# Performance work log

Hardware: AMD Instinct MI355X
Metric: run time of the kernel (lower is better)

## Reference

```python
import jax, jax.numpy as jnp
import numpy as np

N_NODES = 100000
N_EDGES = 1600000
IN_CH, HID, OUT_CH = 512, 16, 64


def setup_inputs() -> dict:
    key = jax.random.key(0)
    ks = jax.random.split(key, 9)
    x = jax.random.normal(ks[0], (N_NODES, IN_CH), dtype=jnp.float32)
    edge_index1 = jax.random.randint(ks[1], (2, N_EDGES), 0, N_NODES, dtype=jnp.int32)
    edge_weight1 = jax.random.uniform(ks[2], (N_EDGES,), dtype=jnp.float32)
    edge_index2 = jax.random.randint(ks[3], (2, N_EDGES), 0, N_NODES, dtype=jnp.int32)
    edge_weight2 = jax.random.uniform(ks[4], (N_EDGES,), dtype=jnp.float32)
    W1 = jax.random.normal(ks[5], (IN_CH, HID), dtype=jnp.float32) / np.sqrt(IN_CH)
    b1 = jnp.zeros((HID,), dtype=jnp.float32)
    W2 = jax.random.normal(ks[6], (HID, OUT_CH), dtype=jnp.float32) / np.sqrt(HID)
    b2 = jnp.zeros((OUT_CH,), dtype=jnp.float32)
    return dict(x=x, edge_index1=edge_index1, edge_weight1=edge_weight1,
                edge_index2=edge_index2, edge_weight2=edge_weight2,
                W1=W1, b1=b1, W2=W2, b2=b2, num_nodes=N_NODES)


def _gcn_conv(x, W, b, row, col, w, num_nodes):
    # symmetric-normalized GCN aggregation: out = D^-1/2 A D^-1/2 (x W) + b
    deg = jax.ops.segment_sum(w, row, num_segments=num_nodes)  # [N]
    dinv = jnp.where(deg > 0, jax.lax.rsqrt(jnp.maximum(deg, 1e-12)), 0.0)
    norm = dinv[row] * w * dinv[col]                            # [E]
    h = x @ W                                                   # [N, F_out]
    msg = norm[:, None] * h[col]                                # [E, F_out]
    return jax.ops.segment_sum(msg, row, num_segments=num_nodes) + b


def reference(x, edge_index1, edge_weight1, edge_index2, edge_weight2,
              W1, b1, W2, b2, num_nodes):
    # concat edge lists; torch_sparse.coalesce(op='add') merges duplicates by
    # summing weights — the subsequent degree + scatter-add aggregation is
    # invariant to that dedup, so we run directly on the concatenated list.
    ei = jnp.concatenate([edge_index1, edge_index2], axis=1)    # [2, 2E]
    ew = jnp.concatenate([edge_weight1, edge_weight2])          # [2E]
    row, col = ei[0], ei[1]
    h = _gcn_conv(x, W1, b1, row, col, ew, num_nodes)
    h = jax.nn.relu(h)  # dropout is identity in eval mode
    h = _gcn_conv(h, W2, b2, row, col, ew, num_nodes)
    return jax.nn.log_softmax(h, axis=1)
```

## Files before the change

### kernel.cpp

```cpp
#include <hip/hip_runtime.h>
#include <hip/hip_bf16.h>

#define IN_CH 512
#define HID 16
#define OUT_CH 64
#define CAP 20480

typedef __attribute__((ext_vector_type(8))) short bf16x8;
typedef __attribute__((ext_vector_type(4))) float f32x4;

__device__ inline unsigned short f2bf(float f) {
    unsigned int u = __float_as_uint(f);
    return (unsigned short)((u + 0x7fffu + ((u >> 16) & 1u)) >> 16);
}

union A8 { bf16x8 v; short2 p[4]; };
__device__ inline short2 pk2(float a, float b) {
    union { __hip_bfloat162 h; short2 s; } u;
    u.h = __float22bfloat162_rn(make_float2(a, b));
    return u.s;
}

__global__ void k_init(int* __restrict__ cursors, int nbk) {
    int i = threadIdx.x;
    if (i < nbk) cursors[i] = i * CAP;
}

__global__ __launch_bounds__(1024) void k_partition(const int* __restrict__ ei1, const float* __restrict__ w1, int E1,
                                                    const int* __restrict__ ei2, const float* __restrict__ w2, int E2,
                                                    int* __restrict__ cursors,
                                                    uint2* __restrict__ packed, int Et) {
    __shared__ int hist[256];
    __shared__ int cur[256];
    int tid = threadIdx.x;
    if (tid < 256) hist[tid] = 0;
    __syncthreads();
    int e0 = blockIdx.x * 16384 + tid;
    #pragma unroll
    for (int j = 0; j < 16; ++j) {
        int e = e0 + j * 1024;
        if (e < Et) {
            int r = (e < E1) ? ei1[e] : ei2[e - E1];
            atomicAdd(&hist[r >> 9], 1);
        }
    }
    __syncthreads();
    if (tid < 256) {
        int h = hist[tid];
        cur[tid] = (h > 0) ? atomicAdd(&cursors[tid], h) : 0;
    }
    __syncthreads();
    #pragma unroll
    for (int j = 0; j < 16; ++j) {
        int e = e0 + j * 1024;
        if (e < Et) {
            int r, c; float w;
            if (e < E1) { r = ei1[e]; c = ei1[e + E1]; w = w1[e]; }
            else        { int f = e - E1; r = ei2[f]; c = ei2[f + E2]; w = w2[f]; }
            int b = r >> 9;
            int pos = atomicAdd(&cur[b], 1);
            packed[pos] = make_uint2(((unsigned)(r & 511) << 17) | (unsigned)c,
                                     __float_as_uint(w));
        }
    }
}

__global__ void k_bucket_scan(const int* __restrict__ cursors, int* __restrict__ cbase, int nbk) {
    __shared__ int s[256];
    int tid = threadIdx.x;
    int v = (tid < nbk) ? (cursors[tid] - tid * CAP) : 0;
    s[tid] = v;
    __syncthreads();
    for (int off = 1; off < 256; off <<= 1) {
        int t = (tid >= off) ? s[tid - off] : 0;
        __syncthreads();
        s[tid] += t;
        __syncthreads();
    }
    if (tid < nbk) cbase[tid] = s[tid] - v;
}

__global__ __launch_bounds__(1024) void k_buildcsr(const uint2* __restrict__ packed,
                                                   const int* __restrict__ cursors,
                                                   const int* __restrict__ cbase,
                                                   int* __restrict__ rowstart, int* __restrict__ cnt,
                                                   float* __restrict__ dinv, int2* __restrict__ csr, int N) {
    __shared__ int lcnt[512];
    __shared__ int lcur[512];
    __shared__ int lscan[512];
    __shared__ float ldeg[512];
    int b = blockIdx.x, tid = threadIdx.x;
    int M = cursors[b] - b * CAP;
    const uint2* pk = packed + (size_t)b * CAP;
    if (tid < 512) { lcnt[tid] = 0; ldeg[tid] = 0.f; }
    __syncthreads();
    for (int i = tid; i < M; i += 1024) atomicAdd(&lcnt[pk[i].x >> 17], 1);
    __syncthreads();
    int v = (tid < 512) ? lcnt[tid] : 0;
    if (tid < 512) lscan[tid] = v;
    __syncthreads();
    for (int off = 1; off < 512; off <<= 1) {
        int t = (tid >= off && tid < 512) ? lscan[tid - off] : 0;
        __syncthreads();
        if (tid < 512) lscan[tid] += t;
        __syncthreads();
    }
    int cb = cbase[b];
    if (tid < 512) {
        int ex = lscan[tid] - v;
        lcur[tid] = cb + ex;
        int node = b * 512 + tid;
        if (node < N) { rowstart[node] = cb + ex; cnt[node] = v; }
    }
    __syncthreads();
    for (int i = tid; i < M; i += 1024) {
        uint2 u = pk[i];
        int lr = u.x >> 17;
        int c  = u.x & 0x1FFFF;
        int p = atomicAdd(&lcur[lr], 1);
        csr[p] = make_int2(c, (int)u.y);
        atomicAdd(&ldeg[lr], __uint_as_float(u.y));
    }
    __syncthreads();
    if (tid < 512) {
        int node = b * 512 + tid;
        if (node < N) {
            float d = ldeg[tid];
            dinv[node] = (d > 0.f) ? rsqrtf(fmaxf(d, 1e-12f)) : 0.f;
        }
    }
}

__global__ void k_prep(const float* __restrict__ W1, unsigned short* __restrict__ W1s) {
    for (int p = threadIdx.x; p < 1024; p += 256) {
        int kc = p >> 6, lane = p & 63;
        int q = lane >> 4, m = lane & 15;
        int k0 = kc * 32 + q * 8;
        unsigned v[8];
        #pragma unroll
        for (int j = 0; j < 8; ++j) v[j] = f2bf(W1[(k0 + j) * HID + m]);
        uint4 o;
        o.x = v[0] | (v[1] << 16); o.y = v[2] | (v[3] << 16);
        o.z = v[4] | (v[5] << 16); o.w = v[6] | (v[7] << 16);
        ((uint4*)W1s)[p] = o;
    }
}

__global__ __launch_bounds__(256) void k_gemm1(const float* __restrict__ x,
                                               const unsigned short* __restrict__ W1s,
                                               const float* __restrict__ dinv,
                                               float* __restrict__ h1s, int n) {
    int wave = threadIdx.x >> 6, lane = threadIdx.x & 63;
    int tiles = (n + 15) >> 4;
    int t = blockIdx.x * 4 + wave;
    if (t >= tiles) return;

    int m = lane & 15, quad = lane >> 4;

    const bf16x8* Wv = (const bf16x8*)W1s;
    bf16x8 Bf[16];
    #pragma unroll
    for (int kc = 0; kc < 16; ++kc) Bf[kc] = Wv[kc * 64 + lane];

    int row = t * 16 + m;
    int rl = min(row, n - 1);
    const float4* xr = (const float4*)(x + (size_t)rl * IN_CH + quad * 8);

    f32x4 acc = {0.f, 0.f, 0.f, 0.f};
    #pragma unroll
    for (int kc = 0; kc < 16; ++kc) {
        float4 v0 = xr[kc * 8];
        float4 v1 = xr[kc * 8 + 1];
        A8 a;
        a.p[0] = pk2(v0.x, v0.y); a.p[1] = pk2(v0.z, v0.w);
        a.p[2] = pk2(v1.x, v1.y); a.p[3] = pk2(v1.z, v1.w);
        acc = __builtin_amdgcn_mfma_f32_16x16x32_bf16(a.v, Bf[kc], acc, 0, 0, 0);
    }

    int base = t * 16 + quad * 4;
    #pragma unroll
    for (int r = 0; r < 4; ++r) {
        int orow = base + r;
        if (orow < n) h1s[(size_t)orow * HID + m] = dinv[orow] * acc[r];
    }
}

__global__ __launch_bounds__(256) void k_agg1(const float* __restrict__ h1s,
                                              const int2* __restrict__ csr,
                                              const int* __restrict__ rowstart,
                                              const int* __restrict__ cnt,
                                              const float* __restrict__ dinv,
                                              const float* __restrict__ b1,
                                              float* __restrict__ out1s, int n) {
    int wave = threadIdx.x >> 6, lane = threadIdx.x & 63;
    int node = blockIdx.x * 4 + wave;
    if (node >= n) return;
    int slot = lane >> 2, c4 = lane & 3;
    const int2* ce = csr + rowstart[node];
    int deg = cnt[node];
    f32x4 acc = {0.f, 0.f, 0.f, 0.f};
    for (int i = slot; i < deg; i += 16) {
        int2 e = ce[i];
        float w = __int_as_float(e.y);
        float4 hv = ((const float4*)(h1s + (size_t)e.x * HID))[c4];
        acc[0] = fmaf(w, hv.x, acc[0]); acc[1] = fmaf(w, hv.y, acc[1]);
        acc[2] = fmaf(w, hv.z, acc[2]); acc[3] = fmaf(w, hv.w, acc[3]);
    }
    #pragma unroll
    for (int off = 4; off < 64; off <<= 1) {
        acc[0] += __shfl_xor(acc[0], off, 64);
        acc[1] += __shfl_xor(acc[1], off, 64);
        acc[2] += __shfl_xor(acc[2], off, 64);
        acc[3] += __shfl_xor(acc[3], off, 64);
    }
    if (lane < 4) {
        float dv = dinv[node];
        float4 bb = ((const float4*)b1)[c4];
        float4 o;
        o.x = fmaxf(fmaf(dv, acc[0], bb.x), 0.f) * dv;
        o.y = fmaxf(fmaf(dv, acc[1], bb.y), 0.f) * dv;
        o.z = fmaxf(fmaf(dv, acc[2], bb.z), 0.f) * dv;
        o.w = fmaxf(fmaf(dv, acc[3], bb.w), 0.f) * dv;
        ((float4*)(out1s + (size_t)node * HID))[c4] = o;
    }
}

__global__ __launch_bounds__(256) void k_layer2(const float* __restrict__ out1s,
                                                const int2* __restrict__ csr,
                                                const int* __restrict__ rowstart,
                                                const int* __restrict__ cnt,
                                                const float* __restrict__ dinv,
                                                const float* __restrict__ W2,
                                                const float* __restrict__ b2,
                                                float* __restrict__ out, int n) {
    __shared__ float W2l[HID * OUT_CH];
    for (int i = threadIdx.x; i < HID * OUT_CH; i += 256) W2l[i] = W2[i];
    __syncthreads();

    int wave = threadIdx.x >> 6, lane = threadIdx.x & 63;
    int node = blockIdx.x * 4 + wave;
    if (node >= n) return;
    int slot = lane >> 2, c4 = lane & 3;
    const int2* ce = csr + rowstart[node];
    int deg = cnt[node];
    f32x4 acc = {0.f, 0.f, 0.f, 0.f};
    for (int i = slot; i < deg; i += 16) {
        int2 e = ce[i];
        float w = __int_as_float(e.y);
        float4 hv = ((const float4*)(out1s + (size_t)e.x * HID))[c4];
        acc[0] = fmaf(w, hv.x, acc[0]); acc[1] = fmaf(w, hv.y, acc[1]);
        acc[2] = fmaf(w, hv.z, acc[2]); acc[3] = fmaf(w, hv.w, acc[3]);
    }
    #pragma unroll
    for (int off = 4; off < 64; off <<= 1) {
        acc[0] += __shfl_xor(acc[0], off, 64);
        acc[1] += __shfl_xor(acc[1], off, 64);
        acc[2] += __shfl_xor(acc[2], off, 64);
        acc[3] += __shfl_xor(acc[3], off, 64);
    }
    float dv = dinv[node];
    acc[0] *= dv; acc[1] *= dv; acc[2] *= dv; acc[3] *= dv;
    float v = b2[lane];
    #pragma unroll
    for (int gg = 0; gg < 4; ++gg) {
        float a0 = __shfl(acc[0], gg, 64);
        float a1 = __shfl(acc[1], gg, 64);
        float a2 = __shfl(acc[2], gg, 64);
        float a3 = __shfl(acc[3], gg, 64);
        v = fmaf(a0, W2l[(4 * gg + 0) * OUT_CH + lane], v);
        v = fmaf(a1, W2l[(4 * gg + 1) * OUT_CH + lane], v);
        v = fmaf(a2, W2l[(4 * gg + 2) * OUT_CH + lane], v);
        v = fmaf(a3, W2l[(4 * gg + 3) * OUT_CH + lane], v);
    }
    float m = v;
    #pragma unroll
    for (int off = 32; off; off >>= 1) m = fmaxf(m, __shfl_xor(m, off, 64));
    float ex = __expf(v - m);
    float s = ex;
    #pragma unroll
    for (int off = 32; off; off >>= 1) s += __shfl_xor(s, off, 64);
    out[(size_t)node * OUT_CH + lane] = (v - m) - __logf(s);
}

extern "C" void kernel_launch(void* const* d_in, const int* in_sizes, int n_in,
                              void* d_out, int out_size, void* d_ws, size_t ws_size,
                              hipStream_t stream) {
    const float* x   = (const float*)d_in[0];
    const int*   ei1 = (const int*)d_in[1];
    const float* w1  = (const float*)d_in[2];
    const int*   ei2 = (const int*)d_in[3];
    const float* w2  = (const float*)d_in[4];
    const float* W1  = (const float*)d_in[5];
    const float* b1  = (const float*)d_in[6];
    const float* W2  = (const float*)d_in[7];
    const float* b2  = (const float*)d_in[8];
    int N  = in_sizes[0] / IN_CH;
    int E1 = in_sizes[2];
    int E2 = in_sizes[4];
    int Et = E1 + E2;
    float* out = (float*)d_out;
    int nbk = (N + 511) >> 9;

    char* p = (char*)d_ws;
    int*   cursors  = (int*)p;   p += 1024;
    int*   cbase    = (int*)p;   p += 1024;
    int*   rowstart = (int*)p;   p += (size_t)N * 4;
    int*   cnt      = (int*)p;   p += (size_t)N * 4;
    float* dinv     = (float*)p; p += (size_t)N * 4;
    unsigned short* W1s = (unsigned short*)p; p += IN_CH * HID * 2;
    int2*  csr      = (int2*)p;  p += (size_t)Et * 8;
    uint2* packed   = (uint2*)p;
    float* h1s      = (float*)p;
    float* out1s    = h1s + (size_t)N * HID;

    k_init<<<1, 256, 0, stream>>>(cursors, nbk);
    k_prep<<<1, 256, 0, stream>>>(W1, W1s);
    k_partition<<<(Et + 16383) / 16384, 1024, 0, stream>>>(ei1, w1, E1, ei2, w2, E2,
                                                           cursors, packed, Et);
    k_bucket_scan<<<1, 256, 0, stream>>>(cursors, cbase, nbk);
    k_buildcsr<<<nbk, 1024, 0, stream>>>(packed, cursors, cbase,
                                         rowstart, cnt, dinv, csr, N);
    int tiles = (N + 15) / 16;
    k_gemm1<<<(tiles + 3) / 4, 256, 0, stream>>>(x, W1s, dinv, h1s, N);
    k_agg1<<<(N + 3) / 4, 256, 0, stream>>>(h1s, csr, rowstart, cnt, dinv, b1, out1s, N);
    k_layer2<<<(N + 3) / 4, 256, 0, stream>>>(out1s, csr, rowstart, cnt, dinv, W2, b2, out, N);
}
```

Baseline: 539.6 us.

## Store hidden features as bf16, merge small kernels, privatize partition histogram

The intermediate hidden features h1s and out1s are now stored as bf16, which halves gather traffic in both aggregation kernels. Those kernels now use 2 lanes per edge and 32 edge slots per wave. The init and W1 prep kernels become one launch, and the bucket scan is folded into every buildcsr block, removing two launches. The partition kernel uses per-256-thread histograms and caches row indices in registers so they are not reloaded. The bf16 storage lowers accuracy of intermediates, and every buildcsr block now repeats the bucket scan.

```diff
diff --git a/kernel.cpp b/kernel.cpp
--- a/kernel.cpp
+++ b/kernel.cpp
@@ -13,6 +13,8 @@
     unsigned int u = __float_as_uint(f);
     return (unsigned short)((u + 0x7fffu + ((u >> 16) & 1u)) >> 16);
 }
+__device__ inline float blo(unsigned u) { return __uint_as_float(u << 16); }
+__device__ inline float bhi(unsigned u) { return __uint_as_float(u & 0xFFFF0000u); }
 
 union A8 { bf16x8 v; short2 p[4]; };
 __device__ inline short2 pk2(float a, float b) {
@@ -21,70 +23,76 @@
     return u.s;
 }
 
-__global__ void k_init(int* __restrict__ cursors, int nbk) {
-    int i = threadIdx.x;
-    if (i < nbk) cursors[i] = i * CAP;
+__global__ void k_init_prep(int* __restrict__ cursors, int nbk,
+                            const float* __restrict__ W1, unsigned short* __restrict__ W1s) {
+    if (blockIdx.x == 0) {
+        int i = threadIdx.x;
+        if (i < nbk) cursors[i] = i * CAP;
+    } else {
+        for (int p = threadIdx.x; p < 1024; p += 256) {
+            int kc = p >> 6, lane = p & 63;
+            int q = lane >> 4, m = lane & 15;
+            int k0 = kc * 32 + q * 8;
+            unsigned v[8];
+            #pragma unroll
+            for (int j = 0; j < 8; ++j) v[j] = f2bf(W1[(k0 + j) * HID + m]);
+            uint4 o;
+            o.x = v[0] | (v[1] << 16); o.y = v[2] | (v[3] << 16);
+            o.z = v[4] | (v[5] << 16); o.w = v[6] | (v[7] << 16);
+            ((uint4*)W1s)[p] = o;
+        }
+    }
 }
 
 __global__ __launch_bounds__(1024) void k_partition(const int* __restrict__ ei1, const float* __restrict__ w1, int E1,
                                                     const int* __restrict__ ei2, const float* __restrict__ w2, int E2,
                                                     int* __restrict__ cursors,
                                                     uint2* __restrict__ packed, int Et) {
-    __shared__ int hist[256];
+    __shared__ int hist[4][256];
     __shared__ int cur[256];
     int tid = threadIdx.x;
-    if (tid < 256) hist[tid] = 0;
+    int wg = tid >> 8;
+    if (tid < 256) { hist[0][tid] = 0; hist[1][tid] = 0; hist[2][tid] = 0; hist[3][tid] = 0; }
     __syncthreads();
     int e0 = blockIdx.x * 16384 + tid;
+    int rr[16];
     #pragma unroll
     for (int j = 0; j < 16; ++j) {
         int e = e0 + j * 1024;
+        rr[j] = -1;
         if (e < Et) {
             int r = (e < E1) ? ei1[e] : ei2[e - E1];
-            atomicAdd(&hist[r >> 9], 1);
+            rr[j] = r;
+            atomicAdd(&hist[wg][r >> 9], 1);
         }
     }
     __syncthreads();
     if (tid < 256) {
-        int h = hist[tid];
+        int h = hist[0][tid] + hist[1][tid] + hist[2][tid] + hist[3][tid];
         cur[tid] = (h > 0) ? atomicAdd(&cursors[tid], h) : 0;
     }
     __syncthreads();
     #pragma unroll
     for (int j = 0; j < 16; ++j) {
         int e = e0 + j * 1024;
-        if (e < Et) {
-            int r, c; float w;
-            if (e < E1) { r = ei1[e]; c = ei1[e + E1]; w = w1[e]; }
-            else        { int f = e - E1; r = ei2[f]; c = ei2[f + E2]; w = w2[f]; }
-            int b = r >> 9;
+        if (rr[j] >= 0) {
+            int c; float w;
+            if (e < E1) { c = ei1[e + E1]; w = w1[e]; }
+            else        { int f = e - E1; c = ei2[f + E2]; w = w2[f]; }
+            int b = rr[j] >> 9;
             int pos = atomicAdd(&cur[b], 1);
-            packed[pos] = make_uint2(((unsigned)(r & 511) << 17) | (unsigned)c,
+            packed[pos] = make_uint2(((unsigned)(rr[j] & 511) << 17) | (unsigned)c,
                                      __float_as_uint(w));
         }
     }
-}
-
-__global__ void k_bucket_scan(const int* __restrict__ cursors, int* __restrict__ cbase, int nbk) {
-    __shared__ int s[256];
-    int tid = threadIdx.x;
-    int v = (tid < nbk) ? (cursors[tid] - tid * CAP) : 0;
-    s[tid] = v;
-    __syncthreads();
-    for (int off = 1; off < 256; off <<= 1) {
-        int t = (tid >= off) ? s[tid - off] : 0;
-        __syncthreads();
-        s[tid] += t;
-        __syncthreads();
-    }
-    if (tid < nbk) cbase[tid] = s[tid] - v;
 }
 
 __global__ __launch_bounds__(1024) void k_buildcsr(const uint2* __restrict__ packed,
                                                    const int* __restrict__ cursors,
-                                                   const int* __restrict__ cbase,
                                                    int* __restrict__ rowstart, int* __restrict__ cnt,
-                                                   float* __restrict__ dinv, int2* __restrict__ csr, int N) {
+                                                   float* __restrict__ dinv, int2* __restrict__ csr,
+                                                   int N, int nbk) {
+    __shared__ int bsc[256];
     __shared__ int lcnt[512];
     __shared__ int lcur[512];
     __shared__ int lscan[512];
@@ -93,7 +101,14 @@
     int M = cursors[b] - b * CAP;
     const uint2* pk = packed + (size_t)b * CAP;
     if (tid < 512) { lcnt[tid] = 0; ldeg[tid] = 0.f; }
-    __syncthreads();
+    if (tid < 256) bsc[tid] = (tid < nbk) ? (cursors[tid] - tid * CAP) : 0;
+    __syncthreads();
+    for (int off = 1; off < 256; off <<= 1) {
+        int t = (tid >= off && tid < 256) ? bsc[tid - off] : 0;
+        __syncthreads();
+        if (tid < 256) bsc[tid] += t;
+        __syncthreads();
+    }
     for (int i = tid; i < M; i += 1024) atomicAdd(&lcnt[pk[i].x >> 17], 1);
     __syncthreads();
     int v = (tid < 512) ? lcnt[tid] : 0;
@@ -105,7 +120,7 @@
         if (tid < 512) lscan[tid] += t;
         __syncthreads();
     }
-    int cb = cbase[b];
+    int cb = (b == 0) ? 0 : bsc[b - 1];
     if (tid < 512) {
         int ex = lscan[tid] - v;
         lcur[tid] = cb + ex;
@@ -131,25 +146,10 @@
     }
 }
 
-__global__ void k_prep(const float* __restrict__ W1, unsigned short* __restrict__ W1s) {
-    for (int p = threadIdx.x; p < 1024; p += 256) {
-        int kc = p >> 6, lane = p & 63;
-        int q = lane >> 4, m = lane & 15;
-        int k0 = kc * 32 + q * 8;
-        unsigned v[8];
-        #pragma unroll
-        for (int j = 0; j < 8; ++j) v[j] = f2bf(W1[(k0 + j) * HID + m]);
-        uint4 o;
-        o.x = v[0] | (v[1] << 16); o.y = v[2] | (v[3] << 16);
-        o.z = v[4] | (v[5] << 16); o.w = v[6] | (v[7] << 16);
-        ((uint4*)W1s)[p] = o;
-    }
-}
-
 __global__ __launch_bounds__(256) void k_gemm1(const float* __restrict__ x,
                                                const unsigned short* __restrict__ W1s,
                                                const float* __restrict__ dinv,
-                                               float* __restrict__ h1s, int n) {
+                                               unsigned short* __restrict__ h1s, int n) {
     int wave = threadIdx.x >> 6, lane = threadIdx.x & 63;
     int tiles = (n + 15) >> 4;
     int t = blockIdx.x * 4 + wave;
@@ -181,51 +181,54 @@
     #pragma unroll
     for (int r = 0; r < 4; ++r) {
         int orow = base + r;
-        if (orow < n) h1s[(size_t)orow * HID + m] = dinv[orow] * acc[r];
-    }
-}
-
-__global__ __launch_bounds__(256) void k_agg1(const float* __restrict__ h1s,
+        if (orow < n) h1s[(size_t)orow * HID + m] = f2bf(dinv[orow] * acc[r]);
+    }
+}
+
+__global__ __launch_bounds__(256) void k_agg1(const unsigned* __restrict__ h1s,
                                               const int2* __restrict__ csr,
                                               const int* __restrict__ rowstart,
                                               const int* __restrict__ cnt,
                                               const float* __restrict__ dinv,
                                               const float* __restrict__ b1,
-                                              float* __restrict__ out1s, int n) {
+                                              unsigned* __restrict__ out1s, int n) {
     int wave = threadIdx.x >> 6, lane = threadIdx.x & 63;
     int node = blockIdx.x * 4 + wave;
     if (node >= n) return;
-    int slot = lane >> 2, c4 = lane & 3;
+    int slot = lane >> 1, c8 = lane & 1;
     const int2* ce = csr + rowstart[node];
     int deg = cnt[node];
-    f32x4 acc = {0.f, 0.f, 0.f, 0.f};
-    for (int i = slot; i < deg; i += 16) {
+    float acc[8] = {0.f,0.f,0.f,0.f,0.f,0.f,0.f,0.f};
+    for (int i = slot; i < deg; i += 32) {
         int2 e = ce[i];
         float w = __int_as_float(e.y);
-        float4 hv = ((const float4*)(h1s + (size_t)e.x * HID))[c4];
-        acc[0] = fmaf(w, hv.x, acc[0]); acc[1] = fmaf(w, hv.y, acc[1]);
-        acc[2] = fmaf(w, hv.z, acc[2]); acc[3] = fmaf(w, hv.w, acc[3]);
-    }
-    #pragma unroll
-    for (int off = 4; off < 64; off <<= 1) {
-        acc[0] += __shfl_xor(acc[0], off, 64);
-        acc[1] += __shfl_xor(acc[1], off, 64);
-        acc[2] += __shfl_xor(acc[2], off, 64);
-        acc[3] += __shfl_xor(acc[3], off, 64);
-    }
-    if (lane < 4) {
+        uint4 hv = ((const uint4*)(h1s + (size_t)e.x * 8))[c8];
+        acc[0] = fmaf(w, blo(hv.x), acc[0]); acc[1] = fmaf(w, bhi(hv.x), acc[1]);
+        acc[2] = fmaf(w, blo(hv.y), acc[2]); acc[3] = fmaf(w, bhi(hv.y), acc[3]);
+        acc[4] = fmaf(w, blo(hv.z), acc[4]); acc[5] = fmaf(w, bhi(hv.z), acc[5]);
+        acc[6] = fmaf(w, blo(hv.w), acc[6]); acc[7] = fmaf(w, bhi(hv.w), acc[7]);
+    }
+    #pragma unroll
+    for (int off = 2; off < 64; off <<= 1) {
+        #pragma unroll
+        for (int j = 0; j < 8; ++j) acc[j] += __shfl_xor(acc[j], off, 64);
+    }
+    if (lane < 2) {
         float dv = dinv[node];
-        float4 bb = ((const float4*)b1)[c4];
-        float4 o;
-        o.x = fmaxf(fmaf(dv, acc[0], bb.x), 0.f) * dv;
-        o.y = fmaxf(fmaf(dv, acc[1], bb.y), 0.f) * dv;
-        o.z = fmaxf(fmaf(dv, acc[2], bb.z), 0.f) * dv;
-        o.w = fmaxf(fmaf(dv, acc[3], bb.w), 0.f) * dv;
-        ((float4*)(out1s + (size_t)node * HID))[c4] = o;
-    }
-}
-
-__global__ __launch_bounds__(256) void k_layer2(const float* __restrict__ out1s,
+        unsigned o[4];
+        #pragma unroll
+        for (int j = 0; j < 4; ++j) {
+            float v0 = fmaxf(fmaf(dv, acc[2*j],   b1[c8*8 + 2*j]),   0.f) * dv;
+            float v1 = fmaxf(fmaf(dv, acc[2*j+1], b1[c8*8 + 2*j+1]), 0.f) * dv;
+            short2 s = pk2(v0, v1);
+            o[j] = (unsigned short)s.x | ((unsigned)(unsigned short)s.y << 16);
+        }
+        uint4 ov = make_uint4(o[0], o[1], o[2], o[3]);
+        ((uint4*)(out1s + (size_t)node * 8))[c8] = ov;
+    }
+}
+
+__global__ __launch_bounds__(256) void k_layer2(const unsigned* __restrict__ out1s,
                                                 const int2* __restrict__ csr,
                                                 const int* __restrict__ rowstart,
                                                 const int* __restrict__ cnt,
@@ -240,37 +243,32 @@
     int wave = threadIdx.x >> 6, lane = threadIdx.x & 63;
     int node = blockIdx.x * 4 + wave;
     if (node >= n) return;
-    int slot = lane >> 2, c4 = lane & 3;
+    int slot = lane >> 1, c8 = lane & 1;
     const int2* ce = csr + rowstart[node];
     int deg = cnt[node];
-    f32x4 acc = {0.f, 0.f, 0.f, 0.f};
-    for (int i = slot; i < deg; i += 16) {
+    float acc[8] = {0.f,0.f,0.f,0.f,0.f,0.f,0.f,0.f};
+    for (int i = slot; i < deg; i += 32) {
         int2 e = ce[i];
         float w = __int_as_float(e.y);
-        float4 hv = ((const float4*)(out1s + (size_t)e.x * HID))[c4];
-        acc[0] = fmaf(w, hv.x, acc[0]); acc[1] = fmaf(w, hv.y, acc[1]);
-        acc[2] = fmaf(w, hv.z, acc[2]); acc[3] = fmaf(w, hv.w, acc[3]);
-    }
-    #pragma unroll
-    for (int off = 4; off < 64; off <<= 1) {
-        acc[0] += __shfl_xor(acc[0], off, 64);
-        acc[1] += __shfl_xor(acc[1], off, 64);
-        acc[2] += __shfl_xor(acc[2], off, 64);
-        acc[3] += __shfl_xor(acc[3], off, 64);
+        uint4 hv = ((const uint4*)(out1s + (size_t)e.x * 8))[c8];
+        acc[0] = fmaf(w, blo(hv.x), acc[0]); acc[1] = fmaf(w, bhi(hv.x), acc[1]);
+        acc[2] = fmaf(w, blo(hv.y), acc[2]); acc[3] = fmaf(w, bhi(hv.y), acc[3]);
+        acc[4] = fmaf(w, blo(hv.z), acc[4]); acc[5] = fmaf(w, bhi(hv.z), acc[5]);
+        acc[6] = fmaf(w, blo(hv.w), acc[6]); acc[7] = fmaf(w, bhi(hv.w), acc[7]);
+    }
+    #pragma unroll
+    for (int off = 2; off < 64; off <<= 1) {
+        #pragma unroll
+        for (int j = 0; j < 8; ++j) acc[j] += __shfl_xor(acc[j], off, 64);
     }
     float dv = dinv[node];
-    acc[0] *= dv; acc[1] *= dv; acc[2] *= dv; acc[3] *= dv;
     float v = b2[lane];
     #pragma unroll
-    for (int gg = 0; gg < 4; ++gg) {
-        float a0 = __shfl(acc[0], gg, 64);
-        float a1 = __shfl(acc[1], gg, 64);
-        float a2 = __shfl(acc[2], gg, 64);
-        float a3 = __shfl(acc[3], gg, 64);
-        v = fmaf(a0, W2l[(4 * gg + 0) * OUT_CH + lane], v);
-        v = fmaf(a1, W2l[(4 * gg + 1) * OUT_CH + lane], v);
-        v = fmaf(a2, W2l[(4 * gg + 2) * OUT_CH + lane], v);
-        v = fmaf(a3, W2l[(4 * gg + 3) * OUT_CH + lane], v);
+    for (int k = 0; k < 8; ++k) {
+        float a0 = __shfl(acc[k], 0, 64) * dv;
+        float a1 = __shfl(acc[k], 1, 64) * dv;
+        v = fmaf(a0, W2l[k * OUT_CH + lane], v);
+        v = fmaf(a1, W2l[(8 + k) * OUT_CH + lane], v);
     }
     float m = v;
     #pragma unroll
@@ -303,25 +301,23 @@
 
     char* p = (char*)d_ws;
     int*   cursors  = (int*)p;   p += 1024;
-    int*   cbase    = (int*)p;   p += 1024;
     int*   rowstart = (int*)p;   p += (size_t)N * 4;
     int*   cnt      = (int*)p;   p += (size_t)N * 4;
     float* dinv     = (float*)p; p += (size_t)N * 4;
     unsigned short* W1s = (unsigned short*)p; p += IN_CH * HID * 2;
     int2*  csr      = (int2*)p;  p += (size_t)Et * 8;
     uint2* packed   = (uint2*)p;
-    float* h1s      = (float*)p;
-    float* out1s    = h1s + (size_t)N * HID;
-
-    k_init<<<1, 256, 0, stream>>>(cursors, nbk);
-    k_prep<<<1, 256, 0, stream>>>(W1, W1s);
+    unsigned short* h1s = (unsigned short*)p;
+    unsigned short* out1s = h1s + (size_t)N * HID;
+
+    k_init_prep<<<2, 256, 0, stream>>>(cursors, nbk, W1, W1s);
     k_partition<<<(Et + 16383) / 16384, 1024, 0, stream>>>(ei1, w1, E1, ei2, w2, E2,
                                                            cursors, packed, Et);
-    k_bucket_scan<<<1, 256, 0, stream>>>(cursors, cbase, nbk);
-    k_buildcsr<<<nbk, 1024, 0, stream>>>(packed, cursors, cbase,
-                                         rowstart, cnt, dinv, csr, N);
+    k_buildcsr<<<nbk, 1024, 0, stream>>>(packed, cursors, rowstart, cnt, dinv, csr, N, nbk);
     int tiles = (N + 15) / 16;
     k_gemm1<<<(tiles + 3) / 4, 256, 0, stream>>>(x, W1s, dinv, h1s, N);
-    k_agg1<<<(N + 3) / 4, 256, 0, stream>>>(h1s, csr, rowstart, cnt, dinv, b1, out1s, N);
-    k_layer2<<<(N + 3) / 4, 256, 0, stream>>>(out1s, csr, rowstart, cnt, dinv, W2, b2, out, N);
-}
+    k_agg1<<<(N + 3) / 4, 256, 0, stream>>>((const unsigned*)h1s, csr, rowstart, cnt, dinv, b1,
+                                            (unsigned*)out1s, N);
+    k_layer2<<<(N + 3) / 4, 256, 0, stream>>>((const unsigned*)out1s, csr, rowstart, cnt, dinv,
+                                              W2, b2, out, N);
+}
```

Result: no change. 541.7 us (+0.4%).
